# Performance work log

Measured on AMD Instinct MI355X. Metric: run time of the kernel, lower is better.

## Reference

```python
import jax, jax.numpy as jnp
import numpy as np

N, E, G = 50000, 800000, 1024      # nodes, edges, graphs
NF, R, H, O, B = 32, 4, 64, 16, 2  # node vocab, relations, hidden, output, conv blocks
MAX_DEG = 10                       # PyG MFConv default max_degree


def setup_inputs() -> dict:
    key = jax.random.key(0)
    ks = jax.random.split(key, 32)
    s = 0.05
    inp = {
        "x": jax.random.normal(ks[0], (N, NF), jnp.float32),
        "edge_attr": jax.random.normal(ks[1], (E, R), jnp.float32),
        "edge_index": jax.random.randint(ks[2], (2, E), 0, N),
        "batch_idx": jnp.sort(jax.random.randint(ks[3], (N,), 0, G)),
        "emb": jax.random.normal(ks[4], (NF, H), jnp.float32) * s,
        "lin1_w": jax.random.normal(ks[5], (H, H), jnp.float32) * s,
        "lin1_b": jnp.zeros((H,), jnp.float32),
        "lin2_w": jax.random.normal(ks[6], (H, O), jnp.float32) * s,
        "lin2_b": jnp.zeros((O,), jnp.float32),
    }
    for b in range(B):
        k = 7 + 4 * b
        inp[f"rgcn_w{b}"] = jax.random.normal(ks[k], (R, H, H), jnp.float32) * s
        inp[f"rgcn_root{b}"] = jax.random.normal(ks[k + 1], (H, H), jnp.float32) * s
        inp[f"rgcn_b{b}"] = jnp.zeros((H,), jnp.float32)
        inp[f"mf_wl{b}"] = jax.random.normal(ks[k + 2], (MAX_DEG + 1, H, H), jnp.float32) * s
        inp[f"mf_bl{b}"] = jnp.zeros((MAX_DEG + 1, H), jnp.float32)
        inp[f"mf_wr{b}"] = jax.random.normal(ks[k + 3], (MAX_DEG + 1, H, H), jnp.float32) * s
    return inp


def _rgcn(h, src, tgt, rel, W, Wroot, bias):
    # PyG RGCNConv: per-relation linear transform + per-(node,relation) MEAN aggregation + root + bias.
    hx = jnp.einsum('nh,rho->rno', h, W)            # [R,N,H] transformed features per relation
    m = hx[rel, src]                                # [E,H] per-edge messages
    seg = tgt * R + rel                             # segment id per (target node, relation)
    cnt = jax.ops.segment_sum(jnp.ones((E,), h.dtype), seg, num_segments=N * R)
    inv = jnp.where(cnt > 0, 1.0 / cnt, 0.0)
    agg = jax.ops.segment_sum(m * inv[seg][:, None], tgt, num_segments=N)
    return agg + h @ Wroot + bias


def _mfconv(h, src, tgt, Wl, bl, Wr):
    # PyG MFConv: sum-aggregate neighbors, then degree-indexed linear layers (lin_l has bias, lin_r none).
    deg = jnp.clip(jax.ops.segment_sum(jnp.ones((E,), jnp.int32), tgt, num_segments=N), 0, MAX_DEG)
    agg = jax.ops.segment_sum(h[src], tgt, num_segments=N)   # [N,H]
    out = jnp.zeros_like(h)
    for d in range(MAX_DEG + 1):                    # fixed small set of degree buckets
        mask = (deg == d)[:, None]
        out = out + jnp.where(mask, agg @ Wl[d] + bl[d] + h @ Wr[d], 0.0)
    return out


def reference(x, edge_index, edge_attr, batch_idx, emb,
              rgcn_w0, rgcn_root0, rgcn_b0, mf_wl0, mf_bl0, mf_wr0,
              rgcn_w1, rgcn_root1, rgcn_b1, mf_wl1, mf_bl1, mf_wr1,
              lin1_w, lin1_b, lin2_w, lin2_b):
    src, tgt = edge_index[0], edge_index[1]
    rel = jnp.argmax(edge_attr, axis=-1)
    h = emb[jnp.argmax(x, axis=-1)]                 # node embedding lookup
    blocks = [(rgcn_w0, rgcn_root0, rgcn_b0, mf_wl0, mf_bl0, mf_wr0),
              (rgcn_w1, rgcn_root1, rgcn_b1, mf_wl1, mf_bl1, mf_wr1)]
    for (W, Wro, bi, Wl, bl, Wr) in blocks:
        h = jax.nn.relu(h)
        h = _rgcn(h, src, tgt, rel, W, Wro, bi)
        h = jax.nn.relu(h)
        h = _mfconv(h, src, tgt, Wl, bl, Wr)
    g = jax.ops.segment_sum(h, batch_idx, num_segments=G)   # global add pool
    g = jax.nn.relu(g @ lin1_w + lin1_b)
    return g @ lin2_w + lin2_b
```

## Files before the change

kernel.cpp:

```cpp
#include <hip/hip_runtime.h>
#include <hip/hip_fp16.h>
#include <cstdint>
#include <cstddef>

#define Nn 50000
#define Ne 800000
#define Ng 1024
#define NFd 32
#define Rr 4
#define Hd 64
#define Od 16
#define MAXD 10
#define NSEG (Nn * Rr)
#define SCAN_BLK ((NSEG + 255) / 256)
#define ORDER_SZ (Nn + 176)
#define NB_MF (ORDER_SZ / 16)
#define NB_RG (Nn / 16)
#define NB_RELSEG (Ne / 256)
#define NB_EMBED (Nn / 8)
#define WT_PER_LAYER (Hd * 5 * Hd)
#define MFWT_PER_LAYER ((MAXD + 1) * Hd * 2 * Hd)
#define PREP_TOTAL (2 * WT_PER_LAYER + 2 * MFWT_PER_LAYER)
#define NB_PREP ((PREP_TOTAL + 255) / 256)

typedef _Float16 f16x8 __attribute__((ext_vector_type(8)));
typedef float f32x4 __attribute__((ext_vector_type(4)));

__device__ __forceinline__ float reluf(float v) { return v > 0.f ? v : 0.f; }
__device__ __forceinline__ int rfl(int v) { return __builtin_amdgcn_readfirstlane(v); }

__global__ void k_rel_emb(const float4* __restrict__ ea, const int* __restrict__ eidx,
                          int* __restrict__ seg, int* __restrict__ rank,
                          int* __restrict__ cnt,
                          const float* __restrict__ x, const float* __restrict__ emb,
                          __half* __restrict__ h16,
                          const float* __restrict__ w0, const float* __restrict__ r0,
                          const float* __restrict__ w1, const float* __restrict__ r1,
                          const float* __restrict__ wl0, const float* __restrict__ wr0,
                          const float* __restrict__ wl1, const float* __restrict__ wr1,
                          __half* __restrict__ wt, __half* __restrict__ mfwt) {
    if (blockIdx.x < NB_RELSEG) {
        int e = blockIdx.x * 256 + threadIdx.x;
        float4 a = ea[e];
        int bi = 0; float bv = a.x;
        if (a.y > bv) { bv = a.y; bi = 1; }
        if (a.z > bv) { bv = a.z; bi = 2; }
        if (a.w > bv) { bv = a.w; bi = 3; }
        int s = eidx[Ne + e] * Rr + bi;
        seg[e] = s;
        rank[e] = atomicAdd(&cnt[s], 1);
    } else if (blockIdx.x < NB_RELSEG + NB_EMBED) {
        int wave = ((blockIdx.x - NB_RELSEG) * 256 + threadIdx.x) >> 6;
        int lane = threadIdx.x & 63;
        int h = lane >> 5, q = lane & 31;
        int node = wave * 2 + h;
        float v = x[(size_t)node * NFd + q];
        int idx = q;
        #pragma unroll
        for (int o = 16; o >= 1; o >>= 1) {
            float ov = __shfl_xor(v, o);
            int oi = __shfl_xor(idx, o);
            if (ov > v || (ov == v && oi < idx)) { v = ov; idx = oi; }
        }
        const float2* e2 = (const float2*)(emb + (size_t)idx * Hd);
        float2 ev = e2[q];
        ((__half2*)h16)[(size_t)node * 32 + q] =
            __floats2half2_rn(reluf(ev.x), reluf(ev.y));
    } else {
        int idx = (blockIdx.x - NB_RELSEG - NB_EMBED) * 256 + threadIdx.x;
        if (idx < 2 * WT_PER_LAYER) {
            int b = idx / WT_PER_LAYER;
            int rem = idx % WT_PER_LAYER;
            int c = rem / 320;
            int k = rem % 320;
            const float* W  = b ? w1 : w0;
            const float* Rt = b ? r1 : r0;
            float v = (k < 64) ? Rt[k * Hd + c]
                               : W[((size_t)((k - 64) >> 6)) * Hd * Hd + ((k - 64) & 63) * Hd + c];
            wt[idx] = __float2half(v);
        } else if (idx < PREP_TOTAL) {
            int j = idx - 2 * WT_PER_LAYER;
            int b = j / MFWT_PER_LAYER;
            int rem = j % MFWT_PER_LAYER;
            int d = rem / (Hd * 128);
            int r2 = rem % (Hd * 128);
            int c = r2 / 128;
            int k = r2 % 128;
            const float* Wl = b ? wl1 : wl0;
            const float* Wr = b ? wr1 : wr0;
            float v = (k < 64) ? Wl[(size_t)d * Hd * Hd + k * Hd + c]
                               : Wr[(size_t)d * Hd * Hd + (k - 64) * Hd + c];
            mfwt[j] = __float2half(v);
        }
    }
}

__global__ void k_scan1(const int* __restrict__ cnt, int* __restrict__ off,
                        int* __restrict__ bsum, int* __restrict__ bcnt) {
    __shared__ int s[256];
    __shared__ int hist[16];
    int t = threadIdx.x;
    if (t < 16) hist[t] = 0;
    int idx = blockIdx.x * 256 + t;
    int v = (idx < NSEG) ? cnt[idx] : 0;
    s[t] = v;
    __syncthreads();
    if ((t & 3) == 0 && idx < NSEG) {
        int dsum = s[t] + s[t + 1] + s[t + 2] + s[t + 3];
        atomicAdd(&hist[min(dsum, MAXD)], 1);
    }
    #pragma unroll
    for (int o = 1; o < 256; o <<= 1) {
        int x = (t >= o) ? s[t - o] : 0;
        __syncthreads();
        s[t] += x;
        __syncthreads();
    }
    if (idx < NSEG) off[idx] = s[t] - v;
    if (t == 255) bsum[blockIdx.x] = s[255];
    if (t < 16) {
        int h = hist[t];
        if (h > 0) atomicAdd(&bcnt[t], h);
    }
}

__global__ void k_scan2(int* __restrict__ bsum, const int* __restrict__ bcnt,
                        int* __restrict__ bbase, int* __restrict__ order) {
    __shared__ int s[1024];
    int t = threadIdx.x;
    int v = (t < SCAN_BLK) ? bsum[t] : 0;
    s[t] = v;
    __syncthreads();
    #pragma unroll
    for (int o = 1; o < 1024; o <<= 1) {
        int x = (t >= o) ? s[t - o] : 0;
        __syncthreads();
        s[t] += x;
        __syncthreads();
    }
    if (t < SCAN_BLK) bsum[t] = s[t] - v;
    if (t == 0) {
        int run = 0;
        for (int d = 0; d <= MAXD; d++) {
            int c = bcnt[d];
            bbase[d] = run;
            int pad = (c + 15) & ~15;
            for (int i = c; i < pad; i++) order[run + i] = -1;
            run += pad;
        }
        for (int i = run; i < ORDER_SZ; i++) order[i] = -1;
    }
}

__global__ void k_scan3_bucket(int* __restrict__ off, const int* __restrict__ bsum,
                               const int4* __restrict__ cnt4, const int* __restrict__ bbase,
                               int* __restrict__ bfill, int* __restrict__ order) {
    __shared__ int hist[16];
    __shared__ int base[16];
    int t = threadIdx.x;
    if (t < 16) hist[t] = 0;
    __syncthreads();
    int idx = blockIdx.x * 256 + t;
    if (idx == 0) off[NSEG] = Ne;
    if (idx < NSEG) off[idx] = off[idx] + bsum[blockIdx.x];
    int d = 0, rk = 0;
    bool valid = (idx < Nn);
    if (valid) {
        int4 c = cnt4[idx];
        d = min(c.x + c.y + c.z + c.w, MAXD);
        rk = atomicAdd(&hist[d], 1);
    }
    __syncthreads();
    if (t < 16) {
        int h = hist[t];
        base[t] = (h > 0) ? atomicAdd(&bfill[t], h) : 0;
    }
    __syncthreads();
    if (valid) order[bbase[d] + base[d] + rk] = idx | (d << 20);
}

__global__ void k_scatter(const int* __restrict__ eidx, const int* __restrict__ seg,
                          const int* __restrict__ rank, const int* __restrict__ off,
                          int* __restrict__ sorted_src) {
    int e = blockIdx.x * 256 + threadIdx.x;
    if (e >= Ne) return;
    int pos = off[seg[e]] + rank[e];
    sorted_src[pos] = eidx[e];
}

__global__ __launch_bounds__(256) void k_rgcn_fused(
        const __half* __restrict__ hin16,
        const int* __restrict__ off, const int* __restrict__ ssrc,
        const __half* __restrict__ wt, const float* __restrict__ bias,
        __half* __restrict__ hout16) {
    __shared__ __align__(16) __half alds[16 * 296];
    int tid = threadIdx.x;
    int wv = tid >> 6, lane = tid & 63;
    int h = lane >> 5, q = lane & 31;
    int nblk = rfl(blockIdx.x * 16);
    int n0 = nblk + wv * 4;
    int obv = off[4 * n0 + min(lane, 16)];
    int cntv = __shfl(obv, lane + 1) - obv;
    float ivv = (cntv > 0) ? 1.f / (float)cntv : 0.f;
    int e    = rfl(__shfl(obv, 0));
    int eEnd = rfl(__shfl(obv, 16));
    const __half2* hp = (const __half2*)hin16;

    float ax = 0.f, ay = 0.f;
    float px = 0.f, py = 0.f;
    float vx = 0.f, vy = 0.f;
    int segi = 0;
    int nb = rfl(__shfl(obv, 1));

#define EMIT(SUB) do {                                               \
        float dx = ax - px, dy = ay - py;                            \
        float ox = ((SUB) && h) ? vx : 0.f;                          \
        float oy = ((SUB) && h) ? vy : 0.f;                          \
        dx -= ox; dy -= oy;                                          \
        dx += __shfl_xor(dx, 32); dy += __shfl_xor(dy, 32);          \
        float iv_ = __shfl(ivv, segi);                               \
        if (lane < 32)                                               \
            *(__half2*)&alds[(wv * 4 + (segi >> 2)) * 296            \
                             + (segi & 3) * 72 + 2 * q]              \
                = __floats2half2_rn(dx * iv_, dy * iv_);             \
        px = ax - ox; py = ay - oy;                                  \
        segi++;                                                      \
        nb = (segi < 16) ? rfl(__shfl(obv, segi + 1)) : 0x7fffffff;  \
    } while (0)

#define PSTEP(dj, t0) {                                              \
        while ((t0) == nb) EMIT(0);                                  \
        float2 f_ = __half22float2(dj);                              \
        vx = f_.x; vy = f_.y; ax += f_.x; ay += f_.y;                \
        while ((t0) + 1 == nb) EMIT(1); }

    if (e + 16 <= eEnd) {
        int4 iA = *(const int4*)(ssrc + e);
        int4 iB = *(const int4*)(ssrc + e + 4);
        int4 iC = *(const int4*)(ssrc + e + 8);
        int4 iD = *(const int4*)(ssrc + e + 12);
        while (true) {
            int s0 = h ? iA.y : iA.x;
            int s1 = h ? iA.w : iA.z;
            int s2 = h ? iB.y : iB.x;
            int s3 = h ? iB.w : iB.z;
            int s4 = h ? iC.y : iC.x;
            int s5 = h ? iC.w : iC.z;
            int s6 = h ? iD.y : iD.x;
            int s7 = h ? iD.w : iD.z;
            __half2 d0 = hp[s0 * 32 + q];
            __half2 d1 = hp[s1 * 32 + q];
            __half2 d2 = hp[s2 * 32 + q];
            __half2 d3 = hp[s3 * 32 + q];
            __half2 d4 = hp[s4 * 32 + q];
            __half2 d5 = hp[s5 * 32 + q];
            __half2 d6 = hp[s6 * 32 + q];
            __half2 d7 = hp[s7 * 32 + q];
            int en = e + 16;
            bool more = (en + 16 <= eEnd);
            int4 jA, jB, jC, jD;
            if (more) {
                jA = *(const int4*)(ssrc + en);
                jB = *(const int4*)(ssrc + en + 4);
                jC = *(const int4*)(ssrc + en + 8);
                jD = *(const int4*)(ssrc + en + 12);
            }
            PSTEP(d0, e + 0)  PSTEP(d1, e + 2)  PSTEP(d2, e + 4)  PSTEP(d3, e + 6)
            PSTEP(d4, e + 8)  PSTEP(d5, e + 10) PSTEP(d6, e + 12) PSTEP(d7, e + 14)
            e = en;
            if (!more) break;
            iA = jA; iB = jB; iC = jC; iD = jD;
        }
    }
    for (; e + 2 <= eEnd; e += 2) {
        while (e == nb) EMIT(0);
        int sa = rfl(ssrc[e]), sb = rfl(ssrc[e + 1]);
        int s = h ? sb : sa;
        float2 f = __half22float2(hp[s * 32 + q]);
        vx = f.x; vy = f.y; ax += f.x; ay += f.y;
        while (e + 1 == nb) EMIT(1);
    }
    if (e < eEnd) {
        while (e == nb) EMIT(0);
        int sa = rfl(ssrc[e]);
        float2 f = __half22float2(hp[sa * 32 + q]);
        if (h) { f.x = 0.f; f.y = 0.f; }
        ax += f.x; ay += f.y;
        e++;
    }
    while (segi < 16) EMIT(0);
#undef PSTEP
#undef EMIT

    __syncthreads();

    int rp = lane & 15;
    int g  = lane >> 4;
    const __half* ha = hin16 + (size_t)(nblk + rp) * Hd + 8 * g;
    const __half* ba = wt + (size_t)(wv * 16 + rp) * 320 + 8 * g;
    const __half* aa = alds + rp * 296 + 8 * g;
    f32x4 dacc = {0.f, 0.f, 0.f, 0.f};
    #pragma unroll
    for (int s = 0; s < 10; s++) {
        f16x8 bfrag = *(const f16x8*)(ba + s * 32);
        f16x8 afrag;
        if (s < 2) afrag = *(const f16x8*)(ha + s * 32);
        else       afrag = *(const f16x8*)(aa + ((s - 2) >> 1) * 72 + ((s - 2) & 1) * 32);
        dacc = __builtin_amdgcn_mfma_f32_16x16x32_f16(afrag, bfrag, dacc, 0, 0, 0);
    }
    int c = wv * 16 + rp;
    float bb = bias[c];
    #pragma unroll
    for (int j = 0; j < 4; j++) {
        int row = nblk + g * 4 + j;
        float v = reluf(dacc[j] + bb);
        hout16[(size_t)row * Hd + c] = __float2half(v);
    }
}

__global__ __launch_bounds__(256) void k_mf_fused(
        const __half* __restrict__ hin16,
        const int* __restrict__ off, const int* __restrict__ ssrc,
        const int* __restrict__ order, const __half* __restrict__ mfwt,
        const float* __restrict__ bl,
        float* __restrict__ hout, __half* __restrict__ hout16, int relu_out) {
    __shared__ __align__(16) __half alds[16 * 72];
    int tid = threadIdx.x;
    int wv = tid >> 6, lane = tid & 63;
    int g2 = lane >> 4, q4 = lane & 15;
    int blk = rfl(blockIdx.x * 16);
    int ent0 = rfl(order[blk]);
    if (ent0 < 0) return;
    int d = ent0 >> 20;
    const uint2* hp2 = (const uint2*)hin16;

#define SEL4(v4) ((g2 & 2) ? ((g2 & 1) ? (v4).w : (v4).z) : ((g2 & 1) ? (v4).y : (v4).x))
#define ACC8(dw) { float2 f_ = __half22float2(*(__half2*)&(dw).x);   \
                   float2 g_ = __half22float2(*(__half2*)&(dw).y);   \
                   a0 += f_.x; a1 += f_.y; a2 += g_.x; a3 += g_.y; }

    for (int i = 0; i < 4; i++) {
        int slot = blk + wv * 4 + i;
        int ent = rfl(order[slot]);
        float a0 = 0.f, a1 = 0.f, a2 = 0.f, a3 = 0.f;
        if (ent >= 0) {
            int n = ent & 0xFFFFF;
            int e0 = rfl(off[n * Rr]);
            int e4 = rfl(off[n * Rr + Rr]);
            int e = e0;
            for (; e + 16 <= e4; e += 16) {
                int4 iA = *(const int4*)(ssrc + e);
                int4 iB = *(const int4*)(ssrc + e + 4);
                int4 iC = *(const int4*)(ssrc + e + 8);
                int4 iD = *(const int4*)(ssrc + e + 12);
                int sA = SEL4(iA), sB = SEL4(iB), sC = SEL4(iC), sD = SEL4(iD);
                uint2 dA = hp2[(size_t)sA * 16 + q4];
                uint2 dB = hp2[(size_t)sB * 16 + q4];
                uint2 dC = hp2[(size_t)sC * 16 + q4];
                uint2 dD = hp2[(size_t)sD * 16 + q4];
                ACC8(dA) ACC8(dB) ACC8(dC) ACC8(dD)
            }
            for (; e + 4 <= e4; e += 4) {
                int4 iA = *(const int4*)(ssrc + e);
                int sA = SEL4(iA);
                uint2 dA = hp2[(size_t)sA * 16 + q4];
                ACC8(dA)
            }
            int rem = e4 - e;
            if (rem > 0) {
                int idxe = e + g2;
                int sl = ssrc[(idxe < e4) ? idxe : (e4 - 1)];
                uint2 dA = hp2[(size_t)sl * 16 + q4];
                float2 f = __half22float2(*(__half2*)&dA.x);
                float2 g = __half22float2(*(__half2*)&dA.y);
                if (idxe >= e4) { f.x = 0.f; f.y = 0.f; g.x = 0.f; g.y = 0.f; }
                a0 += f.x; a1 += f.y; a2 += g.x; a3 += g.y;
            }
        }
        a0 += __shfl_xor(a0, 16); a0 += __shfl_xor(a0, 32);
        a1 += __shfl_xor(a1, 16); a1 += __shfl_xor(a1, 32);
        a2 += __shfl_xor(a2, 16); a2 += __shfl_xor(a2, 32);
        a3 += __shfl_xor(a3, 16); a3 += __shfl_xor(a3, 32);
        if (lane < 16) {
            __half2* dst = (__half2*)&alds[(wv * 4 + i) * 72 + 4 * q4];
            dst[0] = __floats2half2_rn(a0, a1);
            dst[1] = __floats2half2_rn(a2, a3);
        }
    }
#undef SEL4
#undef ACC8
    __syncthreads();

    int rp = lane & 15;
    int g  = lane >> 4;
    int entr = order[blk + rp];
    int nr = (entr >= 0) ? (entr & 0xFFFFF) : 0;
    const __half* aa = alds + rp * 72 + 8 * g;
    const __half* ha = hin16 + (size_t)nr * Hd + 8 * g;
    const __half* ba = mfwt + ((size_t)d * Hd + wv * 16 + rp) * 128 + 8 * g;
    f32x4 dacc = {0.f, 0.f, 0.f, 0.f};
    #pragma unroll
    for (int s = 0; s < 4; s++) {
        f16x8 bfrag = *(const f16x8*)(ba + s * 32);
        f16x8 afrag = (s < 2) ? *(const f16x8*)(aa + s * 32)
                              : *(const f16x8*)(ha + (s - 2) * 32);
        dacc = __builtin_amdgcn_mfma_f32_16x16x32_f16(afrag, bfrag, dacc, 0, 0, 0);
    }
    int c = wv * 16 + rp;
    float bb = bl[d * Hd + c];
    #pragma unroll
    for (int j = 0; j < 4; j++) {
        int entw = order[blk + g * 4 + j];
        if (entw >= 0) {
            int n = entw & 0xFFFFF;
            float v = dacc[j] + bb;
            if (relu_out) hout16[(size_t)n * Hd + c] = __float2half(reluf(v));
            else          hout[(size_t)n * Hd + c] = v;
        }
    }
}

__global__ void k_pool(const float* __restrict__ h, const int* __restrict__ batch,
                       float* __restrict__ g) {
    int wave = rfl((blockIdx.x * 256 + threadIdx.x) >> 6);
    int lane = threadIdx.x & 63;
    int n0 = wave * 4;
    if (n0 >= Nn) return;
    int b0 = batch[n0], b1 = batch[n0 + 1], b2 = batch[n0 + 2], b3 = batch[n0 + 3];
    float v0 = h[(size_t)n0 * Hd + lane];
    float v1 = h[(size_t)(n0 + 1) * Hd + lane];
    float v2 = h[(size_t)(n0 + 2) * Hd + lane];
    float v3 = h[(size_t)(n0 + 3) * Hd + lane];
    if (b0 == b1 && b0 == b2 && b0 == b3) {
        unsafeAtomicAdd(&g[(size_t)b0 * Hd + lane], v0 + v1 + v2 + v3);
    } else {
        unsafeAtomicAdd(&g[(size_t)b0 * Hd + lane], v0);
        unsafeAtomicAdd(&g[(size_t)b1 * Hd + lane], v1);
        unsafeAtomicAdd(&g[(size_t)b2 * Hd + lane], v2);
        unsafeAtomicAdd(&g[(size_t)b3 * Hd + lane], v3);
    }
}

__global__ void k_head(const float* __restrict__ g, const float* __restrict__ w1,
                       const float* __restrict__ b1, const float* __restrict__ w2,
                       const float* __restrict__ b2, float* __restrict__ out) {
    __shared__ float t[4][Hd];
    int wv = threadIdx.x >> 6;
    int lane = threadIdx.x & 63;
    int gi = blockIdx.x * 4 + wv;
    float acc = b1[lane];
    for (int k = 0; k < Hd; k++) acc += g[(size_t)gi * Hd + k] * w1[k * Hd + lane];
    t[wv][lane] = reluf(acc);
    __syncthreads();
    if (lane < Od) {
        float o = b2[lane];
        for (int k = 0; k < Hd; k++) o += t[wv][k] * w2[k * Od + lane];
        out[(size_t)gi * Od + lane] = o;
    }
}

extern "C" void kernel_launch(void* const* d_in, const int* in_sizes, int n_in,
                              void* d_out, int out_size, void* d_ws, size_t ws_size,
                              hipStream_t stream) {
    const float* x      = (const float*)d_in[0];
    const float* ea     = (const float*)d_in[1];
    const int*   eidx   = (const int*)d_in[2];
    const int*   batch  = (const int*)d_in[3];
    const float* emb    = (const float*)d_in[4];
    const float* lin1_w = (const float*)d_in[5];
    const float* lin1_b = (const float*)d_in[6];
    const float* lin2_w = (const float*)d_in[7];
    const float* lin2_b = (const float*)d_in[8];
    const float* rgcn_w[2]    = {(const float*)d_in[9],  (const float*)d_in[15]};
    const float* rgcn_root[2] = {(const float*)d_in[10], (const float*)d_in[16]};
    const float* rgcn_b[2]    = {(const float*)d_in[11], (const float*)d_in[17]};
    const float* mf_wl[2]     = {(const float*)d_in[12], (const float*)d_in[18]};
    const float* mf_bl[2]     = {(const float*)d_in[13], (const float*)d_in[19]};
    const float* mf_wr[2]     = {(const float*)d_in[14], (const float*)d_in[20]};

    char* p = (char*)d_ws;
    float* h32   = (float*)p; p += sizeof(float) * (size_t)Nn * Hd;
    __half* h16a = (__half*)p; p += sizeof(__half) * (size_t)Nn * Hd;
    __half* h16b = (__half*)p; p += sizeof(__half) * (size_t)Nn * Hd;
    float* gbuf  = (float*)p; p += sizeof(float) * (size_t)Ng * Hd;
    __half* wt16 = (__half*)p; p += sizeof(__half) * (size_t)2 * WT_PER_LAYER;
    __half* mfwt16 = (__half*)p; p += sizeof(__half) * (size_t)2 * MFWT_PER_LAYER;
    int* seg     = (int*)p;   p += sizeof(int) * (size_t)Ne;
    int* rank    = (int*)p;   p += sizeof(int) * (size_t)Ne;
    int* ssrc    = (int*)p;   p += sizeof(int) * (size_t)Ne;
    int* cnt     = (int*)p;   p += sizeof(int) * (size_t)NSEG;
    int* bcnt    = (int*)p;   p += sizeof(int) * 16;
    int* bfill   = (int*)p;   p += sizeof(int) * 16;
    int* off     = (int*)p;   p += sizeof(int) * (size_t)(NSEG + 1);
    int* bsum    = (int*)p;   p += sizeof(int) * 1024;
    int* bbase   = (int*)p;   p += sizeof(int) * 16;
    int* order   = (int*)p;   p += sizeof(int) * (size_t)ORDER_SZ;

    hipMemsetAsync(cnt, 0, sizeof(int) * ((size_t)NSEG + 32), stream);
    hipMemsetAsync(gbuf, 0, sizeof(float) * (size_t)Ng * Hd, stream);

    k_rel_emb<<<NB_RELSEG + NB_EMBED + NB_PREP, 256, 0, stream>>>(
        (const float4*)ea, eidx, seg, rank, cnt, x, emb, h16a,
        rgcn_w[0], rgcn_root[0], rgcn_w[1], rgcn_root[1],
        mf_wl[0], mf_wr[0], mf_wl[1], mf_wr[1], wt16, mfwt16);
    k_scan1<<<SCAN_BLK, 256, 0, stream>>>(cnt, off, bsum, bcnt);
    k_scan2<<<1, 1024, 0, stream>>>(bsum, bcnt, bbase, order);
    k_scan3_bucket<<<SCAN_BLK, 256, 0, stream>>>(off, bsum, (const int4*)cnt, bbase,
                                                 bfill, order);
    k_scatter<<<Ne / 256, 256, 0, stream>>>(eidx, seg, rank, off, ssrc);

    __half* hin16 = h16a;  __half* hout16 = h16b;
    for (int b = 0; b < 2; b++) {
        k_rgcn_fused<<<NB_RG, 256, 0, stream>>>(hin16, off, ssrc, wt16 + b * WT_PER_LAYER,
                                                rgcn_b[b], hout16);
        k_mf_fused<<<NB_MF, 256, 0, stream>>>(hout16, off, ssrc, order,
                                              mfwt16 + b * MFWT_PER_LAYER, mf_bl[b],
                                              h32, hin16, b == 0 ? 1 : 0);
    }
    k_pool<<<Nn / 16, 256, 0, stream>>>(h32, batch, gbuf);
    k_head<<<Ng / 4, 256, 0, stream>>>(gbuf, lin1_w, lin1_b, lin2_w, lin2_b, (float*)d_out);
}
```

Baseline: 330.4 us.

## Widen RGCN gather unroll and interleave four node gathers in MF kernel

The RGCN edge-gather loop now processes 32 edges per iteration, with a 16-edge tail block, so more independent half2 loads are in flight. The MFConv aggregation no longer walks its four nodes one after another. It gathers all four together in lockstep rounds, with masked FMA accumulation and prefetch of the next index vectors, to raise memory-level parallelism. The trade-offs are higher register pressure and wasted masked loads when node degrees differ. The prefetch may also read index entries past each node's edge range.

```diff
diff --git a/kernel.cpp b/kernel.cpp
--- a/kernel.cpp
+++ b/kernel.cpp
@@ -234,11 +234,15 @@
         vx = f_.x; vy = f_.y; ax += f_.x; ay += f_.y;                \
         while ((t0) + 1 == nb) EMIT(1); }
 
-    if (e + 16 <= eEnd) {
+    if (e + 32 <= eEnd) {
         int4 iA = *(const int4*)(ssrc + e);
         int4 iB = *(const int4*)(ssrc + e + 4);
         int4 iC = *(const int4*)(ssrc + e + 8);
         int4 iD = *(const int4*)(ssrc + e + 12);
+        int4 iE = *(const int4*)(ssrc + e + 16);
+        int4 iF = *(const int4*)(ssrc + e + 20);
+        int4 iG = *(const int4*)(ssrc + e + 24);
+        int4 iH = *(const int4*)(ssrc + e + 28);
         while (true) {
             int s0 = h ? iA.y : iA.x;
             int s1 = h ? iA.w : iA.z;
@@ -248,6 +252,14 @@
             int s5 = h ? iC.w : iC.z;
             int s6 = h ? iD.y : iD.x;
             int s7 = h ? iD.w : iD.z;
+            int s8 = h ? iE.y : iE.x;
+            int s9 = h ? iE.w : iE.z;
+            int sA = h ? iF.y : iF.x;
+            int sB = h ? iF.w : iF.z;
+            int sC = h ? iG.y : iG.x;
+            int sD = h ? iG.w : iG.z;
+            int sE = h ? iH.y : iH.x;
+            int sF = h ? iH.w : iH.z;
             __half2 d0 = hp[s0 * 32 + q];
             __half2 d1 = hp[s1 * 32 + q];
             __half2 d2 = hp[s2 * 32 + q];
@@ -256,21 +268,61 @@
             __half2 d5 = hp[s5 * 32 + q];
             __half2 d6 = hp[s6 * 32 + q];
             __half2 d7 = hp[s7 * 32 + q];
-            int en = e + 16;
-            bool more = (en + 16 <= eEnd);
-            int4 jA, jB, jC, jD;
+            __half2 d8 = hp[s8 * 32 + q];
+            __half2 d9 = hp[s9 * 32 + q];
+            __half2 dA = hp[sA * 32 + q];
+            __half2 dB = hp[sB * 32 + q];
+            __half2 dC = hp[sC * 32 + q];
+            __half2 dD = hp[sD * 32 + q];
+            __half2 dE = hp[sE * 32 + q];
+            __half2 dF = hp[sF * 32 + q];
+            int en = e + 32;
+            bool more = (en + 32 <= eEnd);
+            int4 jA, jB, jC, jD, jE, jF, jG, jH;
             if (more) {
                 jA = *(const int4*)(ssrc + en);
                 jB = *(const int4*)(ssrc + en + 4);
                 jC = *(const int4*)(ssrc + en + 8);
                 jD = *(const int4*)(ssrc + en + 12);
+                jE = *(const int4*)(ssrc + en + 16);
+                jF = *(const int4*)(ssrc + en + 20);
+                jG = *(const int4*)(ssrc + en + 24);
+                jH = *(const int4*)(ssrc + en + 28);
             }
             PSTEP(d0, e + 0)  PSTEP(d1, e + 2)  PSTEP(d2, e + 4)  PSTEP(d3, e + 6)
             PSTEP(d4, e + 8)  PSTEP(d5, e + 10) PSTEP(d6, e + 12) PSTEP(d7, e + 14)
+            PSTEP(d8, e + 16) PSTEP(d9, e + 18) PSTEP(dA, e + 20) PSTEP(dB, e + 22)
+            PSTEP(dC, e + 24) PSTEP(dD, e + 26) PSTEP(dE, e + 28) PSTEP(dF, e + 30)
             e = en;
             if (!more) break;
             iA = jA; iB = jB; iC = jC; iD = jD;
+            iE = jE; iF = jF; iG = jG; iH = jH;
         }
+    }
+    if (e + 16 <= eEnd) {
+        int4 iA = *(const int4*)(ssrc + e);
+        int4 iB = *(const int4*)(ssrc + e + 4);
+        int4 iC = *(const int4*)(ssrc + e + 8);
+        int4 iD = *(const int4*)(ssrc + e + 12);
+        int s0 = h ? iA.y : iA.x;
+        int s1 = h ? iA.w : iA.z;
+        int s2 = h ? iB.y : iB.x;
+        int s3 = h ? iB.w : iB.z;
+        int s4 = h ? iC.y : iC.x;
+        int s5 = h ? iC.w : iC.z;
+        int s6 = h ? iD.y : iD.x;
+        int s7 = h ? iD.w : iD.z;
+        __half2 d0 = hp[s0 * 32 + q];
+        __half2 d1 = hp[s1 * 32 + q];
+        __half2 d2 = hp[s2 * 32 + q];
+        __half2 d3 = hp[s3 * 32 + q];
+        __half2 d4 = hp[s4 * 32 + q];
+        __half2 d5 = hp[s5 * 32 + q];
+        __half2 d6 = hp[s6 * 32 + q];
+        __half2 d7 = hp[s7 * 32 + q];
+        PSTEP(d0, e + 0)  PSTEP(d1, e + 2)  PSTEP(d2, e + 4)  PSTEP(d3, e + 6)
+        PSTEP(d4, e + 8)  PSTEP(d5, e + 10) PSTEP(d6, e + 12) PSTEP(d7, e + 14)
+        e += 16;
     }
     for (; e + 2 <= eEnd; e += 2) {
         while (e == nb) EMIT(0);
@@ -335,60 +387,79 @@
     const uint2* hp2 = (const uint2*)hin16;
 
 #define SEL4(v4) ((g2 & 2) ? ((g2 & 1) ? (v4).w : (v4).z) : ((g2 & 1) ? (v4).y : (v4).x))
-#define ACC8(dw) { float2 f_ = __half22float2(*(__half2*)&(dw).x);   \
-                   float2 g_ = __half22float2(*(__half2*)&(dw).y);   \
-                   a0 += f_.x; a1 += f_.y; a2 += g_.x; a3 += g_.y; }
-
-    for (int i = 0; i < 4; i++) {
-        int slot = blk + wv * 4 + i;
-        int ent = rfl(order[slot]);
-        float a0 = 0.f, a1 = 0.f, a2 = 0.f, a3 = 0.f;
-        if (ent >= 0) {
-            int n = ent & 0xFFFFF;
-            int e0 = rfl(off[n * Rr]);
-            int e4 = rfl(off[n * Rr + Rr]);
-            int e = e0;
-            for (; e + 16 <= e4; e += 16) {
-                int4 iA = *(const int4*)(ssrc + e);
-                int4 iB = *(const int4*)(ssrc + e + 4);
-                int4 iC = *(const int4*)(ssrc + e + 8);
-                int4 iD = *(const int4*)(ssrc + e + 12);
-                int sA = SEL4(iA), sB = SEL4(iB), sC = SEL4(iC), sD = SEL4(iD);
-                uint2 dA = hp2[(size_t)sA * 16 + q4];
-                uint2 dB = hp2[(size_t)sB * 16 + q4];
-                uint2 dC = hp2[(size_t)sC * 16 + q4];
-                uint2 dD = hp2[(size_t)sD * 16 + q4];
-                ACC8(dA) ACC8(dB) ACC8(dC) ACC8(dD)
-            }
-            for (; e + 4 <= e4; e += 4) {
-                int4 iA = *(const int4*)(ssrc + e);
-                int sA = SEL4(iA);
-                uint2 dA = hp2[(size_t)sA * 16 + q4];
-                ACC8(dA)
-            }
-            int rem = e4 - e;
-            if (rem > 0) {
-                int idxe = e + g2;
-                int sl = ssrc[(idxe < e4) ? idxe : (e4 - 1)];
-                uint2 dA = hp2[(size_t)sl * 16 + q4];
-                float2 f = __half22float2(*(__half2*)&dA.x);
-                float2 g = __half22float2(*(__half2*)&dA.y);
-                if (idxe >= e4) { f.x = 0.f; f.y = 0.f; g.x = 0.f; g.y = 0.f; }
-                a0 += f.x; a1 += f.y; a2 += g.x; a3 += g.y;
-            }
-        }
-        a0 += __shfl_xor(a0, 16); a0 += __shfl_xor(a0, 32);
-        a1 += __shfl_xor(a1, 16); a1 += __shfl_xor(a1, 32);
-        a2 += __shfl_xor(a2, 16); a2 += __shfl_xor(a2, 32);
-        a3 += __shfl_xor(a3, 16); a3 += __shfl_xor(a3, 32);
-        if (lane < 16) {
-            __half2* dst = (__half2*)&alds[(wv * 4 + i) * 72 + 4 * q4];
-            dst[0] = __floats2half2_rn(a0, a1);
-            dst[1] = __floats2half2_rn(a2, a3);
-        }
-    }
+
+    int entA = rfl(order[blk + wv * 4 + 0]);
+    int entB = rfl(order[blk + wv * 4 + 1]);
+    int entC = rfl(order[blk + wv * 4 + 2]);
+    int entD = rfl(order[blk + wv * 4 + 3]);
+    int nA = (entA >= 0) ? (entA & 0xFFFFF) : 0;
+    int nB = (entB >= 0) ? (entB & 0xFFFFF) : 0;
+    int nC = (entC >= 0) ? (entC & 0xFFFFF) : 0;
+    int nD = (entD >= 0) ? (entD & 0xFFFFF) : 0;
+    int eA = rfl(off[nA * Rr]);
+    int eB = rfl(off[nB * Rr]);
+    int eC = rfl(off[nC * Rr]);
+    int eD = rfl(off[nD * Rr]);
+    int lenA = (entA >= 0) ? rfl(off[nA * Rr + Rr]) - eA : 0;
+    int lenB = (entB >= 0) ? rfl(off[nB * Rr + Rr]) - eB : 0;
+    int lenC = (entC >= 0) ? rfl(off[nC * Rr + Rr]) - eC : 0;
+    int lenD = (entD >= 0) ? rfl(off[nD * Rr + Rr]) - eD : 0;
+    int rounds = (max(max(lenA, lenB), max(lenC, lenD)) + 3) >> 2;
+
+    float4 accA = {0.f, 0.f, 0.f, 0.f}, accB = {0.f, 0.f, 0.f, 0.f};
+    float4 accC = {0.f, 0.f, 0.f, 0.f}, accD = {0.f, 0.f, 0.f, 0.f};
+
+    int4 ixA = *(const int4*)(ssrc + eA);
+    int4 ixB = *(const int4*)(ssrc + eB);
+    int4 ixC = *(const int4*)(ssrc + eC);
+    int4 ixD = *(const int4*)(ssrc + eD);
+    for (int r = 0; r < rounds; ++r) {
+        int sA = SEL4(ixA), sB = SEL4(ixB), sC = SEL4(ixC), sD = SEL4(ixD);
+        uint2 dA = hp2[(size_t)sA * 16 + q4];
+        uint2 dB = hp2[(size_t)sB * 16 + q4];
+        uint2 dC = hp2[(size_t)sC * 16 + q4];
+        uint2 dD = hp2[(size_t)sD * 16 + q4];
+        int nx = 4 * (r + 1);
+        int4 jxA = *(const int4*)(ssrc + eA + nx);
+        int4 jxB = *(const int4*)(ssrc + eB + nx);
+        int4 jxC = *(const int4*)(ssrc + eC + nx);
+        int4 jxD = *(const int4*)(ssrc + eD + nx);
+        int base = 4 * r + g2;
+        float mA = (base < lenA) ? 1.f : 0.f;
+        float mB = (base < lenB) ? 1.f : 0.f;
+        float mC = (base < lenC) ? 1.f : 0.f;
+        float mD = (base < lenD) ? 1.f : 0.f;
+        float2 fA = __half22float2(*(__half2*)&dA.x);
+        float2 gA = __half22float2(*(__half2*)&dA.y);
+        accA.x = fmaf(mA, fA.x, accA.x); accA.y = fmaf(mA, fA.y, accA.y);
+        accA.z = fmaf(mA, gA.x, accA.z); accA.w = fmaf(mA, gA.y, accA.w);
+        float2 fB = __half22float2(*(__half2*)&dB.x);
+        float2 gB = __half22float2(*(__half2*)&dB.y);
+        accB.x = fmaf(mB, fB.x, accB.x); accB.y = fmaf(mB, fB.y, accB.y);
+        accB.z = fmaf(mB, gB.x, accB.z); accB.w = fmaf(mB, gB.y, accB.w);
+        float2 fC = __half22float2(*(__half2*)&dC.x);
+        float2 gC = __half22float2(*(__half2*)&dC.y);
+        accC.x = fmaf(mC, fC.x, accC.x); accC.y = fmaf(mC, fC.y, accC.y);
+        accC.z = fmaf(mC, gC.x, accC.z); accC.w = fmaf(mC, gC.y, accC.w);
+        float2 fD = __half22float2(*(__half2*)&dD.x);
+        float2 gD = __half22float2(*(__half2*)&dD.y);
+        accD.x = fmaf(mD, fD.x, accD.x); accD.y = fmaf(mD, fD.y, accD.y);
+        accD.z = fmaf(mD, gD.x, accD.z); accD.w = fmaf(mD, gD.y, accD.w);
+        ixA = jxA; ixB = jxB; ixC = jxC; ixD = jxD;
+    }
+
+#define REDW(P, i) {                                                    \
+        P.x += __shfl_xor(P.x, 16); P.x += __shfl_xor(P.x, 32);         \
+        P.y += __shfl_xor(P.y, 16); P.y += __shfl_xor(P.y, 32);         \
+        P.z += __shfl_xor(P.z, 16); P.z += __shfl_xor(P.z, 32);         \
+        P.w += __shfl_xor(P.w, 16); P.w += __shfl_xor(P.w, 32);         \
+        if (lane < 16) {                                                \
+            __half2* dst = (__half2*)&alds[(wv * 4 + (i)) * 72 + 4 * q4]; \
+            dst[0] = __floats2half2_rn(P.x, P.y);                       \
+            dst[1] = __floats2half2_rn(P.z, P.w); } }
+    REDW(accA, 0) REDW(accB, 1) REDW(accC, 2) REDW(accD, 3)
 #undef SEL4
-#undef ACC8
+#undef REDW
     __syncthreads();
 
     int rp = lane & 15;
```

New measurement: 318.2 us. 1.04x faster.
